# Kernel tuning notes

Measured on AMD Instinct MI355X. Metric: run time of the kernel, lower is better.

Reference implementation:

```python
import jax, jax.numpy as jnp
import numpy as np

HIDDEN = 2048
N_HEADS = 16
HEAD_DIM = HIDDEN // N_HEADS
ROPE_THETA = 10000.0
BSZ, SEQ = 2, 2048
NEG_INF = -1e9


def setup_inputs() -> dict:
    key = jax.random.key(0)
    ks = jax.random.split(key, 5)
    scale = 1.0 / np.sqrt(HIDDEN)
    hidden_states = jax.random.normal(ks[0], (BSZ, SEQ, HIDDEN), dtype=jnp.float32)
    Wq = jax.random.normal(ks[1], (HIDDEN, HIDDEN), dtype=jnp.float32) * scale
    Wk = jax.random.normal(ks[2], (HIDDEN, HIDDEN), dtype=jnp.float32) * scale
    Wv = jax.random.normal(ks[3], (HIDDEN, HIDDEN), dtype=jnp.float32) * scale
    Wo = jax.random.normal(ks[4], (HIDDEN, HIDDEN), dtype=jnp.float32) * scale
    # additive causal mask, [1, 1, S, S]
    causal = jnp.triu(jnp.full((SEQ, SEQ), NEG_INF, dtype=jnp.float32), k=1)
    attention_mask = causal[None, None, :, :]
    position_ids = jnp.arange(SEQ, dtype=jnp.int32)
    return {
        "hidden_states": hidden_states,
        "Wq": Wq, "Wk": Wk, "Wv": Wv, "Wo": Wo,
        "attention_mask": attention_mask,
        "position_ids": position_ids,
    }


def _rotate_half(x):
    half = x.shape[-1] // 2
    return jnp.concatenate((-x[..., half:], x[..., :half]), axis=-1)


def _rope_tables(seq_len, position_ids):
    # inv_freq: [head_dim/2]
    inv_freq = 1.0 / (ROPE_THETA ** (jnp.arange(0, HEAD_DIM, 2, dtype=jnp.float32) / HEAD_DIM))
    t = jnp.arange(seq_len, dtype=jnp.float32)
    freqs = t[:, None] * inv_freq[None, :]              # [S, D/2]
    emb = jnp.concatenate((freqs, freqs), axis=-1)      # [S, D]
    cos = jnp.cos(emb)[position_ids]                    # [S, D]
    sin = jnp.sin(emb)[position_ids]
    return cos, sin


def reference(hidden_states, Wq, Wk, Wv, Wo, attention_mask, position_ids):
    b, s, h = hidden_states.shape
    def proj(W):
        return (hidden_states @ W.T).reshape(b, s, N_HEADS, HEAD_DIM).transpose(0, 2, 1, 3)
    q = proj(Wq)  # [B, H, S, D]
    k = proj(Wk)
    v = proj(Wv)
    cos, sin = _rope_tables(s, position_ids)            # [S, D], broadcasts over B,H
    q = q * cos + _rotate_half(q) * sin
    k = k * cos + _rotate_half(k) * sin
    scores = jnp.einsum('bhqd,bhkd->bhqk', q, k) / np.sqrt(HEAD_DIM)
    scores = scores + attention_mask
    w = jax.nn.softmax(scores, axis=-1)
    out = jnp.einsum('bhqk,bhkd->bhqd', w, v)           # [B, H, S, D]
    out = out.transpose(0, 2, 1, 3).reshape(b, s, h)
    return out @ Wo.T
```

## Files before the change

kernel.cpp:

```cpp
#include <hip/hip_runtime.h>
#include <cstdint>
#include <cstddef>

typedef __bf16 bf16;
typedef __bf16 bf16x4 __attribute__((ext_vector_type(4)));
typedef __bf16 bf16x8 __attribute__((ext_vector_type(8)));
typedef float  f32x4  __attribute__((ext_vector_type(4)));
typedef short  s16x4  __attribute__((ext_vector_type(4)));

#define HIDDEN 2048
#define NHEADS 16
#define HDIM   128
#define BSZ    2
#define SEQ    2048
#define BS     (BSZ*SEQ)
#define QKW    (2*HIDDEN)

union b4u { bf16x4 h; s16x4 s; };

__device__ __forceinline__ void async16(const bf16* g, bf16* l) {
    __builtin_amdgcn_global_load_lds(
        (const __attribute__((address_space(1))) unsigned int*)g,
        (__attribute__((address_space(3))) unsigned int*)l, 16, 0, 0);
}

#define BARX()  asm volatile("s_barrier" ::: "memory")
#define VMW(N)  asm volatile("s_waitcnt vmcnt(" #N ")" ::: "memory")

__device__ __forceinline__ float ex2(float x) {
    float r; asm("v_exp_f32 %0, %1" : "=v"(r) : "v"(x)); return r;
}

__global__ __launch_bounds__(256) void cast_all(const float* __restrict__ hs,
                                                const float* __restrict__ Wq,
                                                const float* __restrict__ Wk,
                                                const float* __restrict__ Wv,
                                                const float* __restrict__ Wo,
                                                const int* __restrict__ pos,
                                                bf16* __restrict__ hs_b,
                                                bf16* __restrict__ wqkv,
                                                bf16* __restrict__ wo_b,
                                                float2* __restrict__ tab) {
    int i = blockIdx.x * 256 + threadIdx.x;
    if (i >= 6291456) {
        int j = i - 6291456;
        int s = j >> 6, p = j & 63;
        float t = (float)pos[s];
        float inv = expf(-(float)(2 * p) * (9.2103403719761836f / 128.0f));
        float sn, cs;
        sincosf(t * inv, &sn, &cs);
        tab[j] = make_float2(cs, sn);
        return;
    }
    const float* src; bf16* dst; int off;
    if (i < 2097152) { src = hs; dst = hs_b; off = i; }
    else {
        int j = i - 2097152;
        int r = j >> 20;
        off = j & 1048575;
        if      (r == 0) { src = Wq; dst = wqkv; }
        else if (r == 1) { src = Wk; dst = wqkv + (size_t)4194304; }
        else if (r == 2) { src = Wv; dst = wqkv + (size_t)8388608; }
        else             { src = Wo; dst = wo_b; }
    }
    const float4 v = ((const float4*)src)[off];
    bf16x4 o;
    o.x = (bf16)v.x; o.y = (bf16)v.y; o.z = (bf16)v.z; o.w = (bf16)v.w;
    ((bf16x4*)dst)[off] = o;
}

__device__ __forceinline__ int qk_perm(int n) {
    int wl = n >> 6, j = n & 63;
    return ((wl >> 1) << 7) | ((j >> 5) << 6) | ((wl & 1) << 5) | (j & 31);
}

#define QKV_TILE(T, DOSTAGE, VMN) do {                                          \
    VMW(VMN);                                                                   \
    BARX();                                                                     \
    const bf16* lAr = lA0 + ((T) & 3) * 16384;                                  \
    const bf16* lBr = lB0 + ((T) & 3) * 16384;                                  \
    bf16x8 bfr[4], af[4];                                                       \
    _Pragma("unroll") for (int nf = 0; nf < 4; ++nf)                            \
        bfr[nf] = *(const bf16x8*)(lBr + nf * 512);                             \
    _Pragma("unroll") for (int mf = 0; mf < 4; ++mf)                            \
        af[mf] = *(const bf16x8*)(lAr + mf * 512);                              \
    if (DOSTAGE) {                                                              \
        bf16* dA = smem + (((T) + 3) & 3) * 16384 + w * 512;                    \
        async16(pa0 + ((T) + 3) * 32, dA);                                      \
        async16(pa1 + ((T) + 3) * 32, dA + 4096);                               \
    }                                                                           \
    __builtin_amdgcn_s_setprio(1);                                              \
    _Pragma("unroll") for (int mf = 0; mf < 4; ++mf)                            \
    _Pragma("unroll") for (int nf = 0; nf < 4; ++nf)                            \
        acc[mf][nf] = __builtin_amdgcn_mfma_f32_16x16x32_bf16(                  \
            af[mf], bfr[nf], acc[mf][nf], 0, 0, 0);                             \
    __builtin_amdgcn_s_setprio(0);                                              \
    _Pragma("unroll") for (int mf = 0; mf < 4; ++mf)                            \
        af[mf] = *(const bf16x8*)(lAr + 2048 + mf * 512);                       \
    if (DOSTAGE) {                                                              \
        bf16* dB = smem + (((T) + 3) & 3) * 16384 + 8192 + w * 512;             \
        async16(pb0 + ((T) + 3) * 32, dB);                                      \
        async16(pb1 + ((T) + 3) * 32, dB + 4096);                               \
    }                                                                           \
    __builtin_amdgcn_s_setprio(1);                                              \
    _Pragma("unroll") for (int mf = 0; mf < 4; ++mf)                            \
    _Pragma("unroll") for (int nf = 0; nf < 4; ++nf)                            \
        acc[4 + mf][nf] = __builtin_amdgcn_mfma_f32_16x16x32_bf16(              \
            af[mf], bfr[nf], acc[4 + mf][nf], 0, 0, 0);                         \
    __builtin_amdgcn_s_setprio(0);                                              \
} while (0)

__global__ __launch_bounds__(512, 2) void gemm_qk(const bf16* __restrict__ A,
                                                  const bf16* __restrict__ Bt,
                                                  const float2* __restrict__ tab,
                                                  bf16* __restrict__ qk) {
    __shared__ alignas(16) bf16 smem[65536];

    const int tid  = threadIdx.x;
    const int lane = tid & 63;
    const int w    = tid >> 6;
    const int l15  = lane & 15;
    const int quad = lane >> 4;
    const int wm   = w >> 2;
    const int wn   = w & 3;

    const int raw = blockIdx.x;
    const int kq  = raw >> 3;
    const int mTile = (kq & 15) * 256;
    const int nTile = (2 * (raw & 7) + (kq >> 4)) * 256;

    const int sRow  = w * 16 + (lane >> 2);
    const int sColE = ((lane & 3) * 8) ^ ((lane & 32) ? 16 : 0);
    const bf16* pa0 = A + (size_t)(mTile + sRow) * HIDDEN + sColE;
    const bf16* pa1 = pa0 + (size_t)128 * HIDDEN;
    const int n0 = qk_perm(sRow), n1 = qk_perm(sRow + 128);
    const bf16* pb0 = Bt + (size_t)(nTile + n0) * HIDDEN + sColE;
    const bf16* pb1 = Bt + (size_t)(nTile + n1) * HIDDEN + sColE;

    const int colE = (quad * 8) ^ ((l15 & 8) ? 16 : 0);
    const bf16* lA0 = smem + (wm * 128 + l15) * 32 + colE;
    const bf16* lB0 = smem + 8192 + (wn * 64 + l15) * 32 + colE;

    f32x4 acc[8][4];
#pragma unroll
    for (int i = 0; i < 8; ++i)
#pragma unroll
        for (int j = 0; j < 4; ++j) acc[i][j] = (f32x4){0.f, 0.f, 0.f, 0.f};

#pragma unroll
    for (int tt = 0; tt < 3; ++tt) {
        bf16* dA = smem + tt * 16384 + w * 512;
        async16(pa0 + tt * 32, dA);
        async16(pa1 + tt * 32, dA + 4096);
        async16(pb0 + tt * 32, dA + 8192);
        async16(pb1 + tt * 32, dA + 12288);
    }

#pragma unroll 4
    for (int t = 0; t < 60; ++t) QKV_TILE(t, 1, 8);
    QKV_TILE(60, 1, 8);
    QKV_TILE(61, 0, 8);
    QKV_TILE(62, 0, 4);
    QKV_TILE(63, 0, 0);

    const float qs = (nTile < HIDDEN) ? (0.08838834764831845f * 1.4426950408889634f) : 1.0f;
    const int hbase = nTile + (wn >> 1) * 128 + (wn & 1) * 32;
#pragma unroll
    for (int mf = 0; mf < 8; ++mf)
#pragma unroll
        for (int r = 0; r < 4; ++r) {
            int row = mTile + wm * 128 + mf * 16 + quad * 4 + r;
            int s   = row & (SEQ - 1);
            float2 t0 = tab[s * 64 + (wn & 1) * 32 + l15];
            float2 t1 = tab[s * 64 + (wn & 1) * 32 + 16 + l15];
            size_t rb = (size_t)row * QKW + hbase + l15;
            float lo0 = acc[mf][0][r], hi0 = acc[mf][2][r];
            float lo1 = acc[mf][1][r], hi1 = acc[mf][3][r];
            qk[rb]      = (bf16)((lo0 * t0.x - hi0 * t0.y) * qs);
            qk[rb + 64] = (bf16)((hi0 * t0.x + lo0 * t0.y) * qs);
            qk[rb + 16] = (bf16)((lo1 * t1.x - hi1 * t1.y) * qs);
            qk[rb + 80] = (bf16)((hi1 * t1.x + lo1 * t1.y) * qs);
        }
}

#define OUT_TILE(T, DOSTAGE, VMN) do {                                          \
    VMW(VMN);                                                                   \
    BARX();                                                                     \
    const bf16* lAr = lA0 + ((T) & 3) * 12288;                                  \
    const bf16* lBr = lB0 + ((T) & 3) * 12288;                                  \
    bf16x8 bfr[4], af[4];                                                       \
    _Pragma("unroll") for (int nf = 0; nf < 4; ++nf)                            \
        bfr[nf] = *(const bf16x8*)(lBr + nf * 512);                             \
    _Pragma("unroll") for (int mf = 0; mf < 4; ++mf)                            \
        af[mf] = *(const bf16x8*)(lAr + mf * 512);                              \
    if (DOSTAGE) {                                                              \
        bf16* dS = smem + (((T) + 3) & 3) * 12288 + w * 512;                    \
        async16(pa0 + ((T) + 3) * 32, dS);                                      \
        async16(pb0 + ((T) + 3) * 32, dS + 4096);                               \
        async16(pb1 + ((T) + 3) * 32, dS + 8192);                               \
    }                                                                           \
    __builtin_amdgcn_s_setprio(1);                                              \
    _Pragma("unroll") for (int mf = 0; mf < 4; ++mf)                            \
    _Pragma("unroll") for (int nf = 0; nf < 4; ++nf)                            \
        acc[mf][nf] = __builtin_amdgcn_mfma_f32_16x16x32_bf16(                  \
            af[mf], bfr[nf], acc[mf][nf], 0, 0, 0);                             \
    __builtin_amdgcn_s_setprio(0);                                              \
} while (0)

#define OUT_PROLOGUE()                                                          \
    const int tid  = threadIdx.x;                                               \
    const int lane = tid & 63;                                                  \
    const int w    = tid >> 6;                                                  \
    const int l15  = lane & 15;                                                 \
    const int quad = lane >> 4;                                                 \
    const int wm   = w >> 2;                                                    \
    const int wn   = w & 3;                                                     \
    const int raw = blockIdx.x;                                                 \
    const int mTile = (raw >> 3) * 128;                                         \
    const int nTile = (raw & 7) * 256;                                          \
    const int sRow  = w * 16 + (lane >> 2);                                     \
    const int sColE = ((lane & 3) * 8) ^ ((lane & 32) ? 16 : 0);                \
    const bf16* pa0 = A + (size_t)(mTile + sRow) * HIDDEN + sColE;              \
    const bf16* pb0 = Bt + (size_t)(nTile + sRow) * HIDDEN + sColE;             \
    const bf16* pb1 = pb0 + (size_t)128 * HIDDEN;                               \
    const int colE = (quad * 8) ^ ((l15 & 8) ? 16 : 0);                         \
    const bf16* lA0 = smem + (wm * 64 + l15) * 32 + colE;                       \
    const bf16* lB0 = smem + 4096 + (wn * 64 + l15) * 32 + colE;                \
    f32x4 acc[4][4];                                                            \
    _Pragma("unroll") for (int i = 0; i < 4; ++i)                               \
    _Pragma("unroll") for (int j = 0; j < 4; ++j)                               \
        acc[i][j] = (f32x4){0.f, 0.f, 0.f, 0.f};                                \
    _Pragma("unroll") for (int tt = 0; tt < 3; ++tt) {                          \
        bf16* dS = smem + tt * 12288 + w * 512;                                 \
        async16(pa0 + tt * 32, dS);                                             \
        async16(pb0 + tt * 32, dS + 4096);                                      \
        async16(pb1 + tt * 32, dS + 8192);                                      \
    }                                                                           \
    _Pragma("unroll 4") for (int t = 0; t < 60; ++t) OUT_TILE(t, 1, 6);         \
    OUT_TILE(60, 1, 6);                                                         \
    OUT_TILE(61, 0, 6);                                                         \
    OUT_TILE(62, 0, 3);                                                         \
    OUT_TILE(63, 0, 0);

__global__ __launch_bounds__(512, 2) void gemm_v(const bf16* __restrict__ A,
                                                 const bf16* __restrict__ Bt,
                                                 bf16* __restrict__ vtb) {
    __shared__ alignas(16) bf16 smem[49152];
    OUT_PROLOGUE()
#pragma unroll
    for (int mf = 0; mf < 4; ++mf)
#pragma unroll
        for (int nf = 0; nf < 4; ++nf) {
            int col_v = nTile + wn * 64 + nf * 16 + l15;
            int row0  = mTile + wm * 64 + mf * 16 + quad * 4;
            bf16x4 pk;
#pragma unroll
            for (int r = 0; r < 4; ++r) pk[r] = (bf16)acc[mf][nf][r];
            *(bf16x4*)(vtb + (size_t)col_v * BS + row0) = pk;
        }
}

__global__ __launch_bounds__(512, 2) void gemm_out(const bf16* __restrict__ A,
                                                   const bf16* __restrict__ Bt,
                                                   float* __restrict__ C) {
    __shared__ alignas(16) bf16 smem[49152];
    OUT_PROLOGUE()
#pragma unroll
    for (int mf = 0; mf < 4; ++mf)
#pragma unroll
        for (int nf = 0; nf < 4; ++nf)
#pragma unroll
            for (int r = 0; r < 4; ++r) {
                int row = mTile + wm * 64 + mf * 16 + quad * 4 + r;
                int col = nTile + wn * 64 + nf * 16 + l15;
                C[(size_t)row * HIDDEN + col] = acc[mf][nf][r];
            }
}

__global__ __launch_bounds__(512, 4) void attn_kernel(const bf16* __restrict__ qk,
                                                      const bf16* __restrict__ vt,
                                                      bf16* __restrict__ ao) {
    __shared__ bf16 Kls[2][64 * 128];
    __shared__ bf16 Vls[2][128 * 64];

    const int tid  = threadIdx.x;
    const int lane = tid & 63;
    const int w    = tid >> 6;
    const int l15  = lane & 15;
    const int quad = lane >> 4;
    const int bid  = blockIdx.x;
    const int half = bid >> 8;
    const int idx  = bid & 255;
    const int qb2  = half ? (idx >> 5) : 15 - (idx >> 5);
    const int bh   = idx & 31;
    const int b    = bh >> 4;
    const int h    = bh & 15;
    const int qbase = qb2 * 128;
    const int nt    = 2 * qb2 + 2;
    const size_t seq0 = (size_t)b * SEQ;

    bf16x8 qf[4];
    {
        const bf16* qp = qk + (seq0 + qbase + w * 16 + l15) * QKW + h * HDIM + quad * 8;
#pragma unroll
        for (int ks = 0; ks < 4; ++ks) qf[ks] = *(const bf16x8*)(qp + ks * 32);
    }
#pragma unroll
    for (int ks = 0; ks < 4; ++ks)
        asm volatile("" :: "v"(*(const f32x4*)&qf[ks]));

    f32x4 o[8];
#pragma unroll
    for (int i = 0; i < 8; ++i) o[i] = (f32x4){0.f, 0.f, 0.f, 0.f};
    float m_s = -3e38f, l_s = 0.f;
    const int qg = qbase + w * 16 + l15;

    const int krow = lane >> 4;
    const int kp   = lane & 15;
    const int vrow = lane >> 3;
    const int vp   = lane & 7;
    const int sw   = l15 & 7;

    const bf16* qksrc = qk + seq0 * QKW + HIDDEN + h * HDIM;
    const bf16* vtsrc = vt + (size_t)h * HDIM * BS + seq0;
    int koff[2], voff[2];
#pragma unroll
    for (int i = 0; i < 2; ++i) {
        int c = w * 2 + i;
        int j = c * 4 + krow;
        int c2 = (kp & 8) | ((kp & 7) ^ (j & 7));
        koff[i] = j * QKW + c2 * 8;
        int d = c * 8 + vrow;
        int cv = vp ^ (d & 7);
        voff[i] = d * BS + cv * 8;
    }

    const bf16* kbase[4];
#pragma unroll
    for (int ks = 0; ks < 4; ++ks)
        kbase[ks] = &Kls[0][l15 * 128 + (((ks * 4 + quad) ^ sw) << 3)];
    const bf16* vbase[4];
#pragma unroll
    for (int ni = 0; ni < 4; ++ni)
        vbase[ni] = &Vls[0][l15 * 64 + ((((ni * 2 + (quad >> 1)) ^ sw) << 3) + (quad & 1) * 4)];

#define ATTN_STAGE(T, BUF) do {                                                  \
        const int kb_ = (T) * 64;                                                \
        _Pragma("unroll") for (int i = 0; i < 2; ++i)                            \
            async16(qksrc + (size_t)kb_ * QKW + koff[i],                         \
                    &Kls[BUF][(w * 2 + i) * 512]);                               \
        _Pragma("unroll") for (int i = 0; i < 2; ++i)                            \
            async16(vtsrc + kb_ + voff[i],                                       \
                    &Vls[BUF][(w * 2 + i) * 512]);                               \
    } while (0)

#define ATTN_TILE(T, BUF) do {                                                   \
        if ((T) + 1 < nt) { ATTN_STAGE((T) + 1, (BUF) ^ 1); VMW(4); }            \
        else              { VMW(0); }                                            \
        BARX();                                                                  \
        const int kb = (T) * 64;                                                 \
        f32x4 sa[4];                                                             \
        _Pragma("unroll") for (int ni = 0; ni < 4; ++ni)                         \
            sa[ni] = (f32x4){0.f, 0.f, 0.f, 0.f};                                \
        _Pragma("unroll") for (int ni = 0; ni < 4; ++ni)                         \
        _Pragma("unroll") for (int ks = 0; ks < 4; ++ks) {                       \
            bf16x8 kf = *(const bf16x8*)(kbase[ks] + (BUF) * 8192 + ni * 2048);  \
            sa[ni] = __builtin_amdgcn_mfma_f32_16x16x32_bf16(kf, qf[ks], sa[ni], 0, 0, 0); \
        }                                                                        \
        float rmax = -3e38f;                                                     \
        const bool diag = ((T) >= nt - 2);                                       \
        _Pragma("unroll") for (int ni = 0; ni < 4; ++ni)                         \
        _Pragma("unroll") for (int r = 0; r < 4; ++r) {                          \
            float sv = sa[ni][r];                                                \
            if (diag && (kb + ni * 16 + quad * 4 + r > qg)) sv = -1e30f;         \
            sa[ni][r] = sv;                                                      \
            rmax = fmaxf(rmax, sv);                                              \
        }                                                                        \
        rmax = fmaxf(rmax, __shfl_xor(rmax, 16));                                \
        rmax = fmaxf(rmax, __shfl_xor(rmax, 32));                                \
        if (__ballot(rmax > m_s + 8.f) != 0ull) {                                \
            float mn = fmaxf(m_s, rmax);                                         \
            float al = ex2(m_s - mn);                                            \
            m_s = mn; l_s *= al;                                                 \
            _Pragma("unroll") for (int n2 = 0; n2 < 8; ++n2)                     \
            _Pragma("unroll") for (int r = 0; r < 4; ++r) o[n2][r] *= al;        \
        }                                                                        \
        float rsum = 0.f;                                                        \
        b4u pb[4];                                                               \
        _Pragma("unroll") for (int ni = 0; ni < 4; ++ni)                         \
        _Pragma("unroll") for (int r = 0; r < 4; ++r) {                          \
            float e = ex2(sa[ni][r] - m_s);                                      \
            rsum += e;                                                           \
            pb[ni].h[r] = (bf16)e;                                               \
        }                                                                        \
        rsum += __shfl_xor(rsum, 16);                                            \
        rsum += __shfl_xor(rsum, 32);                                            \
        l_s += rsum;                                                             \
        _Pragma("unroll") for (int n2 = 0; n2 < 8; ++n2)                         \
        _Pragma("unroll") for (int ni = 0; ni < 4; ++ni) {                       \
            b4u vf;                                                              \
            vf.h = *(const bf16x4*)(vbase[ni] + (BUF) * 8192 + n2 * 1024);       \
            o[n2] = __builtin_amdgcn_mfma_f32_16x16x16bf16_1k(vf.s, pb[ni].s, o[n2], 0, 0, 0); \
        }                                                                        \
        BARX();                                                                  \
    } while (0)

    ATTN_STAGE(0, 0);
    for (int t = 0; t < nt; t += 2) {
        ATTN_TILE(t, 0);
        ATTN_TILE(t + 1, 1);
    }
#undef ATTN_TILE
#undef ATTN_STAGE

    const float inv = 1.0f / l_s;
    bf16* op = ao + (seq0 + qg) * HIDDEN + h * HDIM + quad * 4;
#pragma unroll
    for (int n2 = 0; n2 < 8; ++n2) {
        bf16x4 pk;
#pragma unroll
        for (int r = 0; r < 4; ++r) pk[r] = (bf16)(o[n2][r] * inv);
        *(bf16x4*)(op + n2 * 16) = pk;
    }
}

extern "C" void kernel_launch(void* const* d_in, const int* in_sizes, int n_in,
                              void* d_out, int out_size, void* d_ws, size_t ws_size,
                              hipStream_t stream) {
    const float* hs = (const float*)d_in[0];
    const float* Wq = (const float*)d_in[1];
    const float* Wk = (const float*)d_in[2];
    const float* Wv = (const float*)d_in[3];
    const float* Wo = (const float*)d_in[4];
    const int* pos  = (const int*)d_in[6];
    float* out = (float*)d_out;

    bf16* hs_b = (bf16*)d_ws;
    bf16* wqkv = hs_b + (size_t)8388608;
    bf16* wo_b = wqkv + (size_t)12582912;
    bf16* qkb  = wo_b + (size_t)4194304;
    bf16* vtb  = qkb + (size_t)16777216;
    bf16* ao   = vtb + (size_t)8388608;
    float2* tab = (float2*)ao;

    cast_all<<<25088, 256, 0, stream>>>(hs, Wq, Wk, Wv, Wo, pos, hs_b, wqkv, wo_b, tab);
    gemm_qk<<<256, 512, 0, stream>>>(hs_b, wqkv, tab, qkb);
    gemm_v<<<256, 512, 0, stream>>>(hs_b, wqkv + (size_t)8388608, vtb);
    attn_kernel<<<512, 512, 0, stream>>>(qkb, vtb, ao);
    gemm_out<<<256, 512, 0, stream>>>(ao, wo_b, out);
}
```

Measured before the change: 359.4 us.

## Give each attention wave two 16-row query slices, halving block size to 256

```diff
diff --git a/kernel.cpp b/kernel.cpp
--- a/kernel.cpp
+++ b/kernel.cpp
@@ -277,7 +277,7 @@
             }
 }
 
-__global__ __launch_bounds__(512, 4) void attn_kernel(const bf16* __restrict__ qk,
+__global__ __launch_bounds__(256, 2) void attn_kernel(const bf16* __restrict__ qk,
                                                       const bf16* __restrict__ vt,
                                                       bf16* __restrict__ ao) {
     __shared__ bf16 Kls[2][64 * 128];
@@ -299,21 +299,28 @@
     const int nt    = 2 * qb2 + 2;
     const size_t seq0 = (size_t)b * SEQ;
 
-    bf16x8 qf[4];
-    {
-        const bf16* qp = qk + (seq0 + qbase + w * 16 + l15) * QKW + h * HDIM + quad * 8;
-#pragma unroll
-        for (int ks = 0; ks < 4; ++ks) qf[ks] = *(const bf16x8*)(qp + ks * 32);
-    }
-#pragma unroll
-    for (int ks = 0; ks < 4; ++ks)
-        asm volatile("" :: "v"(*(const f32x4*)&qf[ks]));
-
-    f32x4 o[8];
-#pragma unroll
-    for (int i = 0; i < 8; ++i) o[i] = (f32x4){0.f, 0.f, 0.f, 0.f};
-    float m_s = -3e38f, l_s = 0.f;
-    const int qg = qbase + w * 16 + l15;
+    bf16x8 qf[2][4];
+#pragma unroll
+    for (int qs = 0; qs < 2; ++qs) {
+        const bf16* qp = qk + (seq0 + qbase + w * 32 + qs * 16 + l15) * QKW + h * HDIM + quad * 8;
+#pragma unroll
+        for (int ks = 0; ks < 4; ++ks) qf[qs][ks] = *(const bf16x8*)(qp + ks * 32);
+    }
+#pragma unroll
+    for (int qs = 0; qs < 2; ++qs)
+#pragma unroll
+        for (int ks = 0; ks < 4; ++ks)
+            asm volatile("" :: "v"(*(const f32x4*)&qf[qs][ks]));
+
+    f32x4 o[8][2];
+#pragma unroll
+    for (int i = 0; i < 8; ++i)
+#pragma unroll
+        for (int qs = 0; qs < 2; ++qs) o[i][qs] = (f32x4){0.f, 0.f, 0.f, 0.f};
+    float m_s[2] = {-3e38f, -3e38f}, l_s[2] = {0.f, 0.f};
+    int qg[2];
+#pragma unroll
+    for (int qs = 0; qs < 2; ++qs) qg[qs] = qbase + w * 32 + qs * 16 + l15;
 
     const int krow = lane >> 4;
     const int kp   = lane & 15;
@@ -323,10 +330,10 @@
 
     const bf16* qksrc = qk + seq0 * QKW + HIDDEN + h * HDIM;
     const bf16* vtsrc = vt + (size_t)h * HDIM * BS + seq0;
-    int koff[2], voff[2];
-#pragma unroll
-    for (int i = 0; i < 2; ++i) {
-        int c = w * 2 + i;
+    int koff[4], voff[4];
+#pragma unroll
+    for (int i = 0; i < 4; ++i) {
+        int c = w * 4 + i;
         int j = c * 4 + krow;
         int c2 = (kp & 8) | ((kp & 7) ^ (j & 7));
         koff[i] = j * QKW + c2 * 8;
@@ -346,61 +353,66 @@
 
 #define ATTN_STAGE(T, BUF) do {                                                  \
         const int kb_ = (T) * 64;                                                \
-        _Pragma("unroll") for (int i = 0; i < 2; ++i)                            \
+        _Pragma("unroll") for (int i = 0; i < 4; ++i)                            \
             async16(qksrc + (size_t)kb_ * QKW + koff[i],                         \
-                    &Kls[BUF][(w * 2 + i) * 512]);                               \
-        _Pragma("unroll") for (int i = 0; i < 2; ++i)                            \
+                    &Kls[BUF][(w * 4 + i) * 512]);                               \
+        _Pragma("unroll") for (int i = 0; i < 4; ++i)                            \
             async16(vtsrc + kb_ + voff[i],                                       \
-                    &Vls[BUF][(w * 2 + i) * 512]);                               \
+                    &Vls[BUF][(w * 4 + i) * 512]);                               \
     } while (0)
 
 #define ATTN_TILE(T, BUF) do {                                                   \
-        if ((T) + 1 < nt) { ATTN_STAGE((T) + 1, (BUF) ^ 1); VMW(4); }            \
+        if ((T) + 1 < nt) { ATTN_STAGE((T) + 1, (BUF) ^ 1); VMW(8); }            \
         else              { VMW(0); }                                            \
         BARX();                                                                  \
         const int kb = (T) * 64;                                                 \
-        f32x4 sa[4];                                                             \
+        f32x4 sa[4][2];                                                          \
         _Pragma("unroll") for (int ni = 0; ni < 4; ++ni)                         \
-            sa[ni] = (f32x4){0.f, 0.f, 0.f, 0.f};                                \
+        _Pragma("unroll") for (int qs = 0; qs < 2; ++qs)                         \
+            sa[ni][qs] = (f32x4){0.f, 0.f, 0.f, 0.f};                            \
         _Pragma("unroll") for (int ni = 0; ni < 4; ++ni)                         \
         _Pragma("unroll") for (int ks = 0; ks < 4; ++ks) {                       \
             bf16x8 kf = *(const bf16x8*)(kbase[ks] + (BUF) * 8192 + ni * 2048);  \
-            sa[ni] = __builtin_amdgcn_mfma_f32_16x16x32_bf16(kf, qf[ks], sa[ni], 0, 0, 0); \
+            sa[ni][0] = __builtin_amdgcn_mfma_f32_16x16x32_bf16(kf, qf[0][ks], sa[ni][0], 0, 0, 0); \
+            sa[ni][1] = __builtin_amdgcn_mfma_f32_16x16x32_bf16(kf, qf[1][ks], sa[ni][1], 0, 0, 0); \
         }                                                                        \
-        float rmax = -3e38f;                                                     \
         const bool diag = ((T) >= nt - 2);                                       \
-        _Pragma("unroll") for (int ni = 0; ni < 4; ++ni)                         \
-        _Pragma("unroll") for (int r = 0; r < 4; ++r) {                          \
-            float sv = sa[ni][r];                                                \
-            if (diag && (kb + ni * 16 + quad * 4 + r > qg)) sv = -1e30f;         \
-            sa[ni][r] = sv;                                                      \
-            rmax = fmaxf(rmax, sv);                                              \
+        b4u pb[4][2];                                                            \
+        _Pragma("unroll") for (int qs = 0; qs < 2; ++qs) {                       \
+            float rmax = -3e38f;                                                 \
+            _Pragma("unroll") for (int ni = 0; ni < 4; ++ni)                     \
+            _Pragma("unroll") for (int r = 0; r < 4; ++r) {                      \
+                float sv = sa[ni][qs][r];                                        \
+                if (diag && (kb + ni * 16 + quad * 4 + r > qg[qs])) sv = -1e30f; \
+                sa[ni][qs][r] = sv;                                              \
+                rmax = fmaxf(rmax, sv);                                          \
+            }                                                                    \
+            rmax = fmaxf(rmax, __shfl_xor(rmax, 16));                            \
+            rmax = fmaxf(rmax, __shfl_xor(rmax, 32));                            \
+            if (__ballot(rmax > m_s[qs] + 8.f) != 0ull) {                        \
+                float mn = fmaxf(m_s[qs], rmax);                                 \
+                float al = ex2(m_s[qs] - mn);                                    \
+                m_s[qs] = mn; l_s[qs] *= al;                                     \
+                _Pragma("unroll") for (int n2 = 0; n2 < 8; ++n2)                 \
+                _Pragma("unroll") for (int r = 0; r < 4; ++r) o[n2][qs][r] *= al;\
+            }                                                                    \
+            float rsum = 0.f;                                                    \
+            _Pragma("unroll") for (int ni = 0; ni < 4; ++ni)                     \
+            _Pragma("unroll") for (int r = 0; r < 4; ++r) {                      \
+                float e = ex2(sa[ni][qs][r] - m_s[qs]);                          \
+                rsum += e;                                                       \
+                pb[ni][qs].h[r] = (bf16)e;                                       \
+            }                                                                    \
+            rsum += __shfl_xor(rsum, 16);                                        \
+            rsum += __shfl_xor(rsum, 32);                                        \
+            l_s[qs] += rsum;                                                     \
         }                                                                        \
-        rmax = fmaxf(rmax, __shfl_xor(rmax, 16));                                \
-        rmax = fmaxf(rmax, __shfl_xor(rmax, 32));                                \
-        if (__ballot(rmax > m_s + 8.f) != 0ull) {                                \
-            float mn = fmaxf(m_s, rmax);                                         \
-            float al = ex2(m_s - mn);                                            \
-            m_s = mn; l_s *= al;                                                 \
-            _Pragma("unroll") for (int n2 = 0; n2 < 8; ++n2)                     \
-            _Pragma("unroll") for (int r = 0; r < 4; ++r) o[n2][r] *= al;        \
-        }                                                                        \
-        float rsum = 0.f;                                                        \
-        b4u pb[4];                                                               \
-        _Pragma("unroll") for (int ni = 0; ni < 4; ++ni)                         \
-        _Pragma("unroll") for (int r = 0; r < 4; ++r) {                          \
-            float e = ex2(sa[ni][r] - m_s);                                      \
-            rsum += e;                                                           \
-            pb[ni].h[r] = (bf16)e;                                               \
-        }                                                                        \
-        rsum += __shfl_xor(rsum, 16);                                            \
-        rsum += __shfl_xor(rsum, 32);                                            \
-        l_s += rsum;                                                             \
         _Pragma("unroll") for (int n2 = 0; n2 < 8; ++n2)                         \
         _Pragma("unroll") for (int ni = 0; ni < 4; ++ni) {                       \
             b4u vf;                                                              \
             vf.h = *(const bf16x4*)(vbase[ni] + (BUF) * 8192 + n2 * 1024);       \
-            o[n2] = __builtin_amdgcn_mfma_f32_16x16x16bf16_1k(vf.s, pb[ni].s, o[n2], 0, 0, 0); \
+            o[n2][0] = __builtin_amdgcn_mfma_f32_16x16x16bf16_1k(vf.s, pb[ni][0].s, o[n2][0], 0, 0, 0); \
+            o[n2][1] = __builtin_amdgcn_mfma_f32_16x16x16bf16_1k(vf.s, pb[ni][1].s, o[n2][1], 0, 0, 0); \
         }                                                                        \
         BARX();                                                                  \
     } while (0)
@@ -413,14 +425,17 @@
 #undef ATTN_TILE
 #undef ATTN_STAGE
 
-    const float inv = 1.0f / l_s;
-    bf16* op = ao + (seq0 + qg) * HIDDEN + h * HDIM + quad * 4;
-#pragma unroll
-    for (int n2 = 0; n2 < 8; ++n2) {
-        bf16x4 pk;
-#pragma unroll
-        for (int r = 0; r < 4; ++r) pk[r] = (bf16)(o[n2][r] * inv);
-        *(bf16x4*)(op + n2 * 16) = pk;
+#pragma unroll
+    for (int qs = 0; qs < 2; ++qs) {
+        const float inv = 1.0f / l_s[qs];
+        bf16* op = ao + (seq0 + qg[qs]) * HIDDEN + h * HDIM + quad * 4;
+#pragma unroll
+        for (int n2 = 0; n2 < 8; ++n2) {
+            bf16x4 pk;
+#pragma unroll
+            for (int r = 0; r < 4; ++r) pk[r] = (bf16)(o[n2][qs][r] * inv);
+            *(bf16x4*)(op + n2 * 16) = pk;
+        }
     }
 }
 
@@ -446,6 +461,6 @@
     cast_all<<<25088, 256, 0, stream>>>(hs, Wq, Wk, Wv, Wo, pos, hs_b, wqkv, wo_b, tab);
     gemm_qk<<<256, 512, 0, stream>>>(hs_b, wqkv, tab, qkb);
     gemm_v<<<256, 512, 0, stream>>>(hs_b, wqkv + (size_t)8388608, vtb);
-    attn_kernel<<<512, 512, 0, stream>>>(qkb, vtb, ao);
+    attn_kernel<<<512, 256, 0, stream>>>(qkb, vtb, ao);
     gemm_out<<<256, 512, 0, stream>>>(ao, wo_b, out);
 }
```

Measured after the change: 372.5 us. 3.7% more time.
